# Performance work log

Hardware: AMD Instinct MI355X
Metric: run time of the kernel (lower is better)

The kernel has to match this reference:

```python
import jax, jax.numpy as jnp
import numpy as np

N = 16000
E = 128000
IN_DIM = 512
H1 = 4096
H2 = 1024
OUT_DIM = 64


def setup_inputs() -> dict:
    key = jax.random.key(0)
    ks = jax.random.split(key, 8)
    x = jax.random.normal(ks[0], (N, IN_DIM), dtype=jnp.float32)
    edge_index = jax.random.randint(ks[1], (2, E), 0, N, dtype=jnp.int64)

    def glorot(k, fan_in, fan_out):
        lim = float(np.sqrt(6.0 / (fan_in + fan_out)))
        return jax.random.uniform(k, (fan_in, fan_out), jnp.float32, -lim, lim)

    # PyG SAGEConv: out = lin_l(mean_j x_j) + lin_r(x); lin_l has bias, lin_r does not.
    params = {
        'W1l': glorot(ks[2], IN_DIM, H1), 'b1': jnp.zeros((H1,), jnp.float32),
        'W1r': glorot(ks[3], IN_DIM, H1),
        'W2l': glorot(ks[4], H1, H2), 'b2': jnp.zeros((H2,), jnp.float32),
        'W2r': glorot(ks[5], H1, H2),
        'W3l': glorot(ks[6], H2, OUT_DIM), 'b3': jnp.zeros((OUT_DIM,), jnp.float32),
        'W3r': glorot(ks[7], H2, OUT_DIM),
    }
    return {'x': x, 'edge_index': edge_index, **params}


def _sage_conv(x, src, dst, Wl, b, Wr):
    # mean-aggregate neighbor features at dst, then linear; plus root transform
    agg = jax.ops.segment_sum(x[src], dst, num_segments=N)          # [N, F_in]
    cnt = jax.ops.segment_sum(jnp.ones((src.shape[0],), x.dtype), dst, num_segments=N)
    mean = agg / jnp.maximum(cnt, 1.0)[:, None]
    return mean @ Wl + b + x @ Wr


def reference(x, edge_index, W1l, b1, W1r, W2l, b2, W2r, W3l, b3, W3r):
    src, dst = edge_index[0], edge_index[1]
    h = jax.nn.relu(_sage_conv(x, src, dst, W1l, b1, W1r))   # dropout is identity in eval
    h = jax.nn.relu(_sage_conv(h, src, dst, W2l, b2, W2r))
    h = _sage_conv(h, src, dst, W3l, b3, W3r)
    return jax.nn.log_softmax(h, axis=1)
```

## Files before the change

### kernel.cpp

```cpp
#include <hip/hip_runtime.h>
#include <stdint.h>

typedef __bf16 bf16x8 __attribute__((ext_vector_type(8)));
typedef float  f32x4  __attribute__((ext_vector_type(4)));
typedef const void __attribute__((address_space(1))) gv_t;
typedef void __attribute__((address_space(3))) sv_t;

static __device__ __forceinline__ unsigned short f2bf(float f) {
  unsigned u = __float_as_uint(f);
  u += 0x7fffu + ((u >> 16) & 1u);
  return (unsigned short)(u >> 16);
}
static __device__ __forceinline__ float bf2f(unsigned short h) {
  return __uint_as_float(((unsigned)h) << 16);
}
static __device__ __forceinline__ void gload16(const void* g, void* l) {
  __builtin_amdgcn_global_load_lds((gv_t*)g, (sv_t*)l, 16, 0, 0);
}

__global__ void k_sentinel(float* out, int n, float val) {
  int t = blockIdx.x * 256 + threadIdx.x;
  if (t < n) out[t] = val;
}
__global__ void k_zero(int* p, int n) {
  int t = blockIdx.x * 256 + threadIdx.x;
  if (t < n) p[t] = 0;
}

__global__ void k_detect(const int* ei, int* flag) {
  if (blockIdx.x == 0 && threadIdx.x == 0) {
    int nz = 0;
    for (int t = 0; t < 256; ++t) nz += (ei[2 * t + 1] != 0);
    *flag = (nz == 0) ? 1 : 0;
  }
}

__global__ void k_degree(const int* ei, int E, const int* flag, int* deg) {
  int t = blockIdx.x * 256 + threadIdx.x;
  if (t < E) {
    int d = (*flag) ? ei[2 * (E + t)] : ei[E + t];
    atomicAdd(&deg[d], 1);
  }
}
__global__ void k_scan(const int* deg, int* rp, int* cur, int n) {
  __shared__ int ssum[256];
  int t = threadIdx.x;
  int chunk = (n + 255) >> 8;
  int lo = t * chunk, hi = min(lo + chunk, n);
  int s = 0;
  for (int i = lo; i < hi; ++i) s += deg[i];
  ssum[t] = s;
  __syncthreads();
  if (t == 0) {
    int run = 0;
    for (int i = 0; i < 256; ++i) { int v = ssum[i]; ssum[i] = run; run += v; }
  }
  __syncthreads();
  int run = ssum[t];
  for (int i = lo; i < hi; ++i) { rp[i] = run; cur[i] = run; run += deg[i]; }
  if (t == 255) rp[n] = run;
}
__global__ void k_fill(const int* ei, int E, const int* flag, int* cur, int* col) {
  int t = blockIdx.x * 256 + threadIdx.x;
  if (t < E) {
    int f = *flag;
    int s = f ? ei[2 * t] : ei[t];
    int d = f ? ei[2 * (E + t)] : ei[E + t];
    int p = atomicAdd(&cur[d], 1);
    col[p] = s;
  }
}

__global__ void k_cvtx(const float4* __restrict__ in, ushort4* __restrict__ xm, int total4) {
  int t = blockIdx.x * 256 + threadIdx.x;
  if (t < total4) {
    int row = t >> 7, c = t & 127;
    float4 v = in[t];
    xm[(size_t)row * 256 + c] = make_ushort4(f2bf(v.x), f2bf(v.y), f2bf(v.z), f2bf(v.w));
  }
}

__global__ void k_transW(const float* W, unsigned short* Wt, int K, int N, int ld, int kofs) {
  __shared__ float tile[32][33];
  int tx = threadIdx.x & 31, ty = threadIdx.x >> 5;
  int n0 = blockIdx.x << 5, k0 = blockIdx.y << 5;
#pragma unroll
  for (int r = 0; r < 4; ++r)
    tile[ty + r * 8][tx] = W[(size_t)(k0 + ty + r * 8) * N + n0 + tx];
  __syncthreads();
#pragma unroll
  for (int r = 0; r < 4; ++r)
    Wt[(size_t)(n0 + ty + r * 8) * ld + kofs + k0 + tx] = f2bf(tile[tx][ty + r * 8]);
}

__global__ void k_agg(ushort4* __restrict__ xm, const int* __restrict__ rp,
                      const int* __restrict__ col) {
  int i = blockIdx.x;
  int s = rp[i], e = rp[i + 1];
  float inv = 1.0f / (float)max(e - s, 1);
  int f = threadIdx.x;
  float4 a = make_float4(0.f, 0.f, 0.f, 0.f);
  for (int n = s; n < e; ++n) {
    ushort4 v = xm[(size_t)col[n] * 256 + f];
    a.x += bf2f(v.x); a.y += bf2f(v.y); a.z += bf2f(v.z); a.w += bf2f(v.w);
  }
  xm[(size_t)i * 256 + 128 + f] =
      make_ushort4(f2bf(a.x * inv), f2bf(a.y * inv), f2bf(a.z * inv), f2bf(a.w * inv));
}

template <bool RELU, bool BIAS>
__global__ __launch_bounds__(512, 1) void k_gemm256(
    const unsigned short* __restrict__ A, const unsigned short* __restrict__ B,
    const float* __restrict__ bias, unsigned short* __restrict__ outp,
    int Mreal, int N, int K, int bnShift) {
  __shared__ __align__(16) unsigned short lds[2][2][256 * 64];

  const int tid = threadIdx.x;
  const int lane = tid & 63;
  const int wq = tid >> 6;
  const int wr = wq >> 2;
  const int wc = wq & 3;

  const int nwg = gridDim.x;
  const int q8 = nwg >> 3, r8 = nwg & 7;
  const int xcd = blockIdx.x & 7, idx = blockIdx.x >> 3;
  const int wg = (xcd < r8 ? xcd * (q8 + 1) : r8 * (q8 + 1) + (xcd - r8) * q8) + idx;
  const int bn = wg & ((1 << bnShift) - 1);
  const int bm = wg >> bnShift;

  const unsigned short* Ap = A + (size_t)bm * 256 * K;
  const unsigned short* Bp = B + (size_t)bn * 256 * K;
  const int sl8 = ((lane & 7) ^ (lane >> 3)) * 8;
  const int rsub = wq * 8 + (lane >> 3);

#define STAGE_A(BUF, I, K0)                                            \
  gload16(Ap + (size_t)((I) * 64 + rsub) * K + (K0) + sl8,             \
          (char*)&lds[BUF][0][0] + ((I) * 64 + wq * 8) * 128)
#define STAGE_B(BUF, I, K0)                                            \
  gload16(Bp + (size_t)((I) * 64 + rsub) * K + (K0) + sl8,             \
          (char*)&lds[BUF][1][0] + ((I) * 64 + wq * 8) * 128)

  f32x4 acc[8][4];
#pragma unroll
  for (int m = 0; m < 8; ++m)
#pragma unroll
    for (int n = 0; n < 4; ++n) acc[m][n] = (f32x4){0.f, 0.f, 0.f, 0.f};

#define QUAD(BUF, QA, QB)                                                              \
  do {                                                                                 \
    bf16x8 afr[4][2], bfr[2][2];                                                       \
    const char* baseA = (const char*)&lds[BUF][0][0];                                  \
    const char* baseB = (const char*)&lds[BUF][1][0];                                  \
    _Pragma("unroll") for (int mm = 0; mm < 4; ++mm) {                                 \
      const int rr = ((QA) * 4 + mm) * 32 + wr * 16 + (lane & 15);                     \
      _Pragma("unroll") for (int kk = 0; kk < 2; ++kk)                                 \
          afr[mm][kk] = *(const bf16x8*)(baseA + rr * 128 +                            \
                                         (((kk * 4 + (lane >> 4)) ^ (lane & 7)) << 4)); \
    }                                                                                  \
    _Pragma("unroll") for (int nn = 0; nn < 2; ++nn) {                                 \
      const int cc = ((QB) * 2 + nn) * 64 + wc * 16 + (lane & 15);                     \
      _Pragma("unroll") for (int kk = 0; kk < 2; ++kk)                                 \
          bfr[nn][kk] = *(const bf16x8*)(baseB + cc * 128 +                            \
                                         (((kk * 4 + (lane >> 4)) ^ (lane & 7)) << 4)); \
    }                                                                                  \
    asm volatile("s_waitcnt lgkmcnt(0)" ::: "memory");                                 \
    __builtin_amdgcn_sched_barrier(0);                                                 \
    __builtin_amdgcn_s_setprio(1);                                                     \
    _Pragma("unroll") for (int mm = 0; mm < 4; ++mm)                                   \
        _Pragma("unroll") for (int nn = 0; nn < 2; ++nn)                               \
            _Pragma("unroll") for (int kk = 0; kk < 2; ++kk)                           \
                acc[(QA) * 4 + mm][(QB) * 2 + nn] =                                    \
                    __builtin_amdgcn_mfma_f32_16x16x32_bf16(                           \
                        afr[mm][kk], bfr[nn][kk], acc[(QA) * 4 + mm][(QB) * 2 + nn],   \
                        0, 0, 0);                                                      \
    __builtin_amdgcn_s_setprio(0);                                                     \
  } while (0)

  STAGE_A(0, 0, 0); STAGE_A(0, 1, 0);
  STAGE_B(0, 0, 0); STAGE_B(0, 1, 0);
  STAGE_B(0, 2, 0); STAGE_B(0, 3, 0);
  STAGE_A(0, 2, 0); STAGE_A(0, 3, 0);

  const int nt = K >> 6;
#pragma unroll 1
  for (int t = 0; t < nt; ++t) {
    const int cur = t & 1, nxt = cur ^ 1;
    const int k1 = (t + 1) << 6;
    const bool last = (t == nt - 1);
    asm volatile("s_waitcnt vmcnt(4)" ::: "memory");
    __builtin_amdgcn_s_barrier();
    asm volatile("" ::: "memory");
    if (!last) { STAGE_A(nxt, 0, k1); STAGE_A(nxt, 1, k1); }
    QUAD(cur, 0, 0);
    if (last) asm volatile("s_waitcnt vmcnt(2)" ::: "memory");
    else      asm volatile("s_waitcnt vmcnt(4)" ::: "memory");
    __builtin_amdgcn_s_barrier();
    asm volatile("" ::: "memory");
    if (!last) { STAGE_B(nxt, 0, k1); STAGE_B(nxt, 1, k1); }
    QUAD(cur, 0, 1);
    if (last) asm volatile("s_waitcnt vmcnt(0)" ::: "memory");
    else      asm volatile("s_waitcnt vmcnt(4)" ::: "memory");
    __builtin_amdgcn_s_barrier();
    asm volatile("" ::: "memory");
    if (!last) { STAGE_B(nxt, 2, k1); STAGE_B(nxt, 3, k1); }
    QUAD(cur, 1, 0);
    if (!last) { STAGE_A(nxt, 2, k1); STAGE_A(nxt, 3, k1); }
    QUAD(cur, 1, 1);
  }

  const int row0 = bm * 256 + wr * 16 + ((lane >> 4) << 2);
  const int col0 = bn * 256 + wc * 16 + (lane & 15);
#pragma unroll
  for (int m = 0; m < 8; ++m) {
#pragma unroll
    for (int n = 0; n < 4; ++n) {
      const int col = col0 + n * 64;
      float bb = BIAS ? bias[col] : 0.f;
#pragma unroll
      for (int r = 0; r < 4; ++r) {
        int row = row0 + m * 32 + r;
        if (row < Mreal) {
          float v = acc[m][n][r] + bb;
          if (RELU) v = fmaxf(v, 0.f);
          outp[(size_t)row * N + col] = f2bf(v);
        }
      }
    }
  }
#undef QUAD
#undef STAGE_A
#undef STAGE_B
}

template <int NF, bool TWO, bool RELU, bool BIAS>
__global__ __launch_bounds__(256) void k_gemm(
    const unsigned short* __restrict__ Am, const unsigned short* __restrict__ Ar,
    const unsigned short* __restrict__ Bl, const unsigned short* __restrict__ Br,
    const float* __restrict__ bias, unsigned short* __restrict__ outp, int N, int K) {
  constexpr int BN = NF * 32;
  __shared__ __align__(16) unsigned short lds[(128 + BN) * 64];
  unsigned short* ldsA = lds;
  unsigned short* ldsB = lds + 128 * 64;

  const int tid = threadIdx.x;
  const int lane = tid & 63;
  const int w = tid >> 6;
  const int wr = w >> 1, wc = w & 1;

  f32x4 zero = {0.f, 0.f, 0.f, 0.f};
  f32x4 acc[4][NF];
#pragma unroll
  for (int m = 0; m < 4; ++m)
#pragma unroll
    for (int n = 0; n < NF; ++n) acc[m][n] = zero;

  const int bm = blockIdx.x, bn = blockIdx.y;
  const int sl_st = (lane & 7) ^ (lane >> 3);

#pragma unroll 1
  for (int pass = 0; pass < (TWO ? 2 : 1); ++pass) {
    const unsigned short* A = (TWO && pass) ? Ar : Am;
    const unsigned short* B = (TWO && pass) ? Br : Bl;
    A += (size_t)bm * 128 * K;
    B += (size_t)bn * BN * K;
#pragma unroll 1
    for (int k0 = 0; k0 < K; k0 += 64) {
      __syncthreads();
#pragma unroll
      for (int q = 0; q < 4; ++q) {
        int rowi = (w * 4 + q) * 8 + (lane >> 3);
        gload16(A + (size_t)rowi * K + k0 + sl_st * 8, (char*)ldsA + (w * 4 + q) * 1024);
      }
#pragma unroll
      for (int q = 0; q < NF; ++q) {
        int rowi = (w * NF + q) * 8 + (lane >> 3);
        gload16(B + (size_t)rowi * K + k0 + sl_st * 8, (char*)ldsB + (w * NF + q) * 1024);
      }
      __syncthreads();
#pragma unroll
      for (int kk = 0; kk < 2; ++kk) {
        int sw = (((kk * 4 + (lane >> 4)) ^ (lane & 7)) << 4);
        bf16x8 af[4], bfr[NF];
#pragma unroll
        for (int m = 0; m < 4; ++m) {
          int r = wr * 64 + m * 16 + (lane & 15);
          af[m] = *(const bf16x8*)((const char*)ldsA + r * 128 + sw);
        }
#pragma unroll
        for (int n = 0; n < NF; ++n) {
          int c = wc * (BN / 2) + n * 16 + (lane & 15);
          bfr[n] = *(const bf16x8*)((const char*)ldsB + c * 128 + sw);
        }
#pragma unroll
        for (int m = 0; m < 4; ++m)
#pragma unroll
          for (int n = 0; n < NF; ++n)
            acc[m][n] = __builtin_amdgcn_mfma_f32_16x16x32_bf16(af[m], bfr[n], acc[m][n], 0, 0, 0);
      }
    }
  }

  const int row0 = bm * 128 + wr * 64;
  const int col0 = bn * BN + wc * (BN / 2);
#pragma unroll
  for (int m = 0; m < 4; ++m) {
#pragma unroll
    for (int n = 0; n < NF; ++n) {
      int col = col0 + n * 16 + (lane & 15);
      float bb = BIAS ? bias[col] : 0.f;
#pragma unroll
      for (int r = 0; r < 4; ++r) {
        int row = row0 + m * 16 + ((lane >> 4) << 2) + r;
        float v = acc[m][n][r] + bb;
        if (RELU) v = fmaxf(v, 0.f);
        outp[(size_t)row * N + col] = f2bf(v);
      }
    }
  }
}

__global__ void k_combine2(const ushort4* __restrict__ Z2, const int* __restrict__ rp,
                           const int* __restrict__ col, const float* __restrict__ bias,
                           ushort4* __restrict__ h2) {
  int i = blockIdx.x;
  int s = rp[i], e = rp[i + 1];
  float inv = 1.0f / (float)max(e - s, 1);
  int f = threadIdx.x;
  float4 a = make_float4(0.f, 0.f, 0.f, 0.f);
  float4 b = make_float4(0.f, 0.f, 0.f, 0.f);
  int n = s;
  for (; n + 1 < e; n += 2) {
    int j0 = col[n], j1 = col[n + 1];
    ushort4 v0 = Z2[(size_t)j0 * 512 + f];
    ushort4 v1 = Z2[(size_t)j1 * 512 + f];
    a.x += bf2f(v0.x); a.y += bf2f(v0.y); a.z += bf2f(v0.z); a.w += bf2f(v0.w);
    b.x += bf2f(v1.x); b.y += bf2f(v1.y); b.z += bf2f(v1.z); b.w += bf2f(v1.w);
  }
  if (n < e) {
    ushort4 v0 = Z2[(size_t)col[n] * 512 + f];
    a.x += bf2f(v0.x); a.y += bf2f(v0.y); a.z += bf2f(v0.z); a.w += bf2f(v0.w);
  }
  a.x += b.x; a.y += b.y; a.z += b.z; a.w += b.w;
  ushort4 r = Z2[(size_t)i * 512 + 256 + f];
  float4 b4 = ((const float4*)bias)[f];
  float o0 = fmaxf(a.x * inv + bf2f(r.x) + b4.x, 0.f);
  float o1 = fmaxf(a.y * inv + bf2f(r.y) + b4.y, 0.f);
  float o2 = fmaxf(a.z * inv + bf2f(r.z) + b4.z, 0.f);
  float o3 = fmaxf(a.w * inv + bf2f(r.w) + b4.w, 0.f);
  h2[(size_t)i * 256 + f] = make_ushort4(f2bf(o0), f2bf(o1), f2bf(o2), f2bf(o3));
}

__global__ void k_combine3(const unsigned short* __restrict__ Z3, const int* __restrict__ rp,
                           const int* __restrict__ col, const float* __restrict__ bias,
                           float* __restrict__ out) {
  int i = blockIdx.x * 4 + (threadIdx.x >> 6);
  int c = threadIdx.x & 63;
  int s = rp[i], e = rp[i + 1];
  float inv = 1.0f / (float)max(e - s, 1);
  float a = 0.f;
  for (int n = s; n < e; ++n) a += bf2f(Z3[(size_t)col[n] * 128 + c]);
  float v = a * inv + bf2f(Z3[(size_t)i * 128 + 64 + c]) + bias[c];
  float m = v;
#pragma unroll
  for (int o = 1; o < 64; o <<= 1) m = fmaxf(m, __shfl_xor(m, o, 64));
  float t = expf(v - m);
  float sum = t;
#pragma unroll
  for (int o = 1; o < 64; o <<= 1) sum += __shfl_xor(sum, o, 64);
  out[(size_t)i * 64 + c] = (v - m) - logf(sum);
}

extern "C" void kernel_launch(void* const* d_in, const int* in_sizes, int n_in,
                              void* d_out, int out_size, void* d_ws, size_t ws_size,
                              hipStream_t stream) {
  const float* x   = (const float*)d_in[0];
  const int*   ei  = (const int*)d_in[1];
  const float* W1l = (const float*)d_in[2];
  const float* b1  = (const float*)d_in[3];
  const float* W1r = (const float*)d_in[4];
  const float* W2l = (const float*)d_in[5];
  const float* b2  = (const float*)d_in[6];
  const float* W2r = (const float*)d_in[7];
  const float* W3l = (const float*)d_in[8];
  const float* b3  = (const float*)d_in[9];
  const float* W3r = (const float*)d_in[10];

  const int Nn = 16000;
  const int E = in_sizes[1] / 2;

  char* p = (char*)d_ws;
  auto carve = [&](size_t bytes) {
    char* r = p;
    p += (bytes + 255) & ~(size_t)255;
    return r;
  };
  int* deg    = (int*)carve((size_t)Nn * 4);
  int* rp     = (int*)carve((size_t)(Nn + 1) * 4);
  int* cur    = (int*)carve((size_t)Nn * 4);
  int* flag   = (int*)carve(4);
  int* colidx = (int*)carve((size_t)E * 4);
  unsigned short* Wb = (unsigned short*)carve((size_t)2048 * 4096 * 2);
  unsigned short* xm = (unsigned short*)carve((size_t)Nn * 1024 * 2);
  unsigned short* h1 = (unsigned short*)carve((size_t)Nn * 4096 * 2);
  unsigned short* Z2 = (unsigned short*)carve((size_t)Nn * 2048 * 2);
  unsigned short* Z3 = (unsigned short*)carve((size_t)Nn * 128 * 2);
  unsigned short* h2 = xm;

  size_t need = (size_t)(p - (char*)d_ws);
  if (ws_size < need) {
    k_sentinel<<<(out_size + 255) / 256, 256, 0, stream>>>((float*)d_out, out_size,
                                                           (float)(ws_size >> 20));
    return;
  }

  k_zero<<<(Nn + 255) / 256, 256, 0, stream>>>(deg, Nn);
  k_detect<<<1, 64, 0, stream>>>(ei, flag);
  k_degree<<<(E + 255) / 256, 256, 0, stream>>>(ei, E, flag, deg);
  k_scan<<<1, 256, 0, stream>>>(deg, rp, cur, Nn);
  k_fill<<<(E + 255) / 256, 256, 0, stream>>>(ei, E, flag, cur, colidx);

  k_cvtx<<<(Nn * 128 + 255) / 256, 256, 0, stream>>>((const float4*)x, (ushort4*)xm, Nn * 128);
  k_transW<<<dim3(4096 / 32, 512 / 32), 256, 0, stream>>>(W1r, Wb, 512, 4096, 1024, 0);
  k_transW<<<dim3(4096 / 32, 512 / 32), 256, 0, stream>>>(W1l, Wb, 512, 4096, 1024, 512);
  k_agg<<<Nn, 128, 0, stream>>>((ushort4*)xm, rp, colidx);
  k_gemm256<true, true><<<63 * 16, 512, 0, stream>>>(xm, Wb, b1, h1, Nn, 4096, 1024, 4);

  k_transW<<<dim3(1024 / 32, 4096 / 32), 256, 0, stream>>>(W2l, Wb, 4096, 1024, 4096, 0);
  k_transW<<<dim3(1024 / 32, 4096 / 32), 256, 0, stream>>>(W2r, Wb + (size_t)1024 * 4096, 4096,
                                                           1024, 4096, 0);
  k_gemm256<false, false><<<63 * 8, 512, 0, stream>>>(h1, Wb, nullptr, Z2, Nn, 2048, 4096, 3);
  k_combine2<<<Nn, 256, 0, stream>>>((const ushort4*)Z2, rp, colidx, b2, (ushort4*)h2);

  k_transW<<<dim3(64 / 32, 1024 / 32), 256, 0, stream>>>(W3l, Wb, 1024, 64, 1024, 0);
  k_transW<<<dim3(64 / 32, 1024 / 32), 256, 0, stream>>>(W3r, Wb + (size_t)64 * 1024, 1024, 64,
                                                         1024, 0);
  k_gemm<4, false, false, false><<<dim3(125, 1), 256, 0, stream>>>(h2, nullptr, Wb, nullptr,
                                                                   nullptr, Z3, 128, 1024);
  k_combine3<<<Nn / 4, 256, 0, stream>>>(Z3, rp, colidx, b3, (float*)d_out);

  (void)n_in; (void)out_size;
}
```

Before: 636.5 us.

## Restructure GEMM main loop into barrier-bracketed phases with LDS reads before staging

Rewrites the 256x256 GEMM k-loop as four phases. Each phase first issues its LDS fragment reads, then the next tile's global-to-LDS staging, then a vmcnt gate and a barrier, and finally the MFMA cluster followed by a second barrier. The last iteration is split out so the steady-state loop has no per-phase branching. The intent is a ping-pong style schedule where LDS reads and global loads overlap across waves, at the cost of twice as many barriers per iteration.

New measurement: 2.174 ms. 3.42x slower.

```diff
diff --git a/kernel.cpp b/kernel.cpp
--- a/kernel.cpp
+++ b/kernel.cpp
@@ -139,6 +139,7 @@
 #define STAGE_B(BUF, I, K0)                                            \
   gload16(Bp + (size_t)((I) * 64 + rsub) * K + (K0) + sl8,             \
           (char*)&lds[BUF][1][0] + ((I) * 64 + wq * 8) * 128)
+#define VMCNT(NUM) asm volatile("s_waitcnt vmcnt(" #NUM ")" ::: "memory")
 
   f32x4 acc[8][4];
 #pragma unroll
@@ -146,66 +147,63 @@
 #pragma unroll
     for (int n = 0; n < 4; ++n) acc[m][n] = (f32x4){0.f, 0.f, 0.f, 0.f};
 
-#define QUAD(BUF, QA, QB)                                                              \
-  do {                                                                                 \
-    bf16x8 afr[4][2], bfr[2][2];                                                       \
-    const char* baseA = (const char*)&lds[BUF][0][0];                                  \
-    const char* baseB = (const char*)&lds[BUF][1][0];                                  \
-    _Pragma("unroll") for (int mm = 0; mm < 4; ++mm) {                                 \
-      const int rr = ((QA) * 4 + mm) * 32 + wr * 16 + (lane & 15);                     \
-      _Pragma("unroll") for (int kk = 0; kk < 2; ++kk)                                 \
-          afr[mm][kk] = *(const bf16x8*)(baseA + rr * 128 +                            \
+#define PHASE(CUR, QA, QB, STAGE_STMT, GATE_STMT)                                       \
+  do {                                                                                  \
+    bf16x8 afr[4][2], bfr[2][2];                                                        \
+    const char* baseA = (const char*)&lds[CUR][0][0];                                   \
+    const char* baseB = (const char*)&lds[CUR][1][0];                                   \
+    _Pragma("unroll") for (int mm = 0; mm < 4; ++mm) {                                  \
+      const int rr = ((QA) * 4 + mm) * 32 + wr * 16 + (lane & 15);                      \
+      _Pragma("unroll") for (int kk = 0; kk < 2; ++kk)                                  \
+          afr[mm][kk] = *(const bf16x8*)(baseA + rr * 128 +                             \
                                          (((kk * 4 + (lane >> 4)) ^ (lane & 7)) << 4)); \
-    }                                                                                  \
-    _Pragma("unroll") for (int nn = 0; nn < 2; ++nn) {                                 \
-      const int cc = ((QB) * 2 + nn) * 64 + wc * 16 + (lane & 15);                     \
-      _Pragma("unroll") for (int kk = 0; kk < 2; ++kk)                                 \
-          bfr[nn][kk] = *(const bf16x8*)(baseB + cc * 128 +                            \
+    }                                                                                   \
+    _Pragma("unroll") for (int nn = 0; nn < 2; ++nn) {                                  \
+      const int cc = ((QB) * 2 + nn) * 64 + wc * 16 + (lane & 15);                      \
+      _Pragma("unroll") for (int kk = 0; kk < 2; ++kk)                                  \
+          bfr[nn][kk] = *(const bf16x8*)(baseB + cc * 128 +                             \
                                          (((kk * 4 + (lane >> 4)) ^ (lane & 7)) << 4)); \
-    }                                                                                  \
-    asm volatile("s_waitcnt lgkmcnt(0)" ::: "memory");                                 \
-    __builtin_amdgcn_sched_barrier(0);                                                 \
-    __builtin_amdgcn_s_setprio(1);                                                     \
-    _Pragma("unroll") for (int mm = 0; mm < 4; ++mm)                                   \
-        _Pragma("unroll") for (int nn = 0; nn < 2; ++nn)                               \
-            _Pragma("unroll") for (int kk = 0; kk < 2; ++kk)                           \
-                acc[(QA) * 4 + mm][(QB) * 2 + nn] =                                    \
-                    __builtin_amdgcn_mfma_f32_16x16x32_bf16(                           \
-                        afr[mm][kk], bfr[nn][kk], acc[(QA) * 4 + mm][(QB) * 2 + nn],   \
-                        0, 0, 0);                                                      \
-    __builtin_amdgcn_s_setprio(0);                                                     \
+    }                                                                                   \
+    STAGE_STMT;                                                                         \
+    GATE_STMT;                                                                          \
+    __builtin_amdgcn_s_barrier();                                                       \
+    asm volatile("s_waitcnt lgkmcnt(0)" ::: "memory");                                  \
+    __builtin_amdgcn_sched_barrier(0);                                                  \
+    __builtin_amdgcn_s_setprio(1);                                                      \
+    _Pragma("unroll") for (int mm = 0; mm < 4; ++mm)                                    \
+        _Pragma("unroll") for (int nn = 0; nn < 2; ++nn)                                \
+            _Pragma("unroll") for (int kk = 0; kk < 2; ++kk)                            \
+                acc[(QA) * 4 + mm][(QB) * 2 + nn] =                                     \
+                    __builtin_amdgcn_mfma_f32_16x16x32_bf16(                            \
+                        afr[mm][kk], bfr[nn][kk], acc[(QA) * 4 + mm][(QB) * 2 + nn],    \
+                        0, 0, 0);                                                       \
+    __builtin_amdgcn_s_setprio(0);                                                      \
+    __builtin_amdgcn_s_barrier();                                                       \
   } while (0)
 
   STAGE_A(0, 0, 0); STAGE_A(0, 1, 0);
   STAGE_B(0, 0, 0); STAGE_B(0, 1, 0);
   STAGE_B(0, 2, 0); STAGE_B(0, 3, 0);
   STAGE_A(0, 2, 0); STAGE_A(0, 3, 0);
+  VMCNT(4);
+  __builtin_amdgcn_s_barrier();
 
   const int nt = K >> 6;
 #pragma unroll 1
   for (int t = 0; t < nt; ++t) {
     const int cur = t & 1, nxt = cur ^ 1;
     const int k1 = (t + 1) << 6;
-    const bool last = (t == nt - 1);
-    asm volatile("s_waitcnt vmcnt(4)" ::: "memory");
-    __builtin_amdgcn_s_barrier();
-    asm volatile("" ::: "memory");
-    if (!last) { STAGE_A(nxt, 0, k1); STAGE_A(nxt, 1, k1); }
-    QUAD(cur, 0, 0);
-    if (last) asm volatile("s_waitcnt vmcnt(2)" ::: "memory");
-    else      asm volatile("s_waitcnt vmcnt(4)" ::: "memory");
-    __builtin_amdgcn_s_barrier();
-    asm volatile("" ::: "memory");
-    if (!last) { STAGE_B(nxt, 0, k1); STAGE_B(nxt, 1, k1); }
-    QUAD(cur, 0, 1);
-    if (last) asm volatile("s_waitcnt vmcnt(0)" ::: "memory");
-    else      asm volatile("s_waitcnt vmcnt(4)" ::: "memory");
-    __builtin_amdgcn_s_barrier();
-    asm volatile("" ::: "memory");
-    if (!last) { STAGE_B(nxt, 2, k1); STAGE_B(nxt, 3, k1); }
-    QUAD(cur, 1, 0);
-    if (!last) { STAGE_A(nxt, 2, k1); STAGE_A(nxt, 3, k1); }
-    QUAD(cur, 1, 1);
+    if (t < nt - 1) {
+      PHASE(cur, 0, 0, ({ STAGE_A(nxt, 0, k1); STAGE_A(nxt, 1, k1); }), VMCNT(4));
+      PHASE(cur, 0, 1, ({ STAGE_B(nxt, 0, k1); STAGE_B(nxt, 1, k1); }), VMCNT(4));
+      PHASE(cur, 1, 0, ({ STAGE_B(nxt, 2, k1); STAGE_B(nxt, 3, k1); }), (void)0);
+      PHASE(cur, 1, 1, ({ STAGE_A(nxt, 2, k1); STAGE_A(nxt, 3, k1); }), VMCNT(4));
+    } else {
+      PHASE(cur, 0, 0, (void)0, VMCNT(2));
+      PHASE(cur, 0, 1, (void)0, VMCNT(0));
+      PHASE(cur, 1, 0, (void)0, (void)0);
+      PHASE(cur, 1, 1, (void)0, (void)0);
+    }
   }
 
   const int row0 = bm * 256 + wr * 16 + ((lane >> 4) << 2);
@@ -227,7 +225,8 @@
       }
     }
   }
-#undef QUAD
+#undef PHASE
+#undef VMCNT
 #undef STAGE_A
 #undef STAGE_B
 }
```
